# Optimization experiments

Hardware: AMD Instinct MI355X
Metric: run time of the kernel (lower is better)

Reference implementation:

```python
import jax, jax.numpy as jnp
import numpy as np

B, S, H = 1, 2048, 1024
NH, NKV, HD = 16, 4, 64  # n_attn_heads, n_kv_heads, head_dim


def setup_inputs() -> dict:
    key = jax.random.key(0)
    k1, k2, k3, k4 = jax.random.split(key, 4)
    x = jax.random.normal(k1, (B, S, H), dtype=jnp.float32)
    Wq = jax.random.normal(k2, (H, H), dtype=jnp.float32) * 0.02
    Wk = jax.random.normal(k3, (NKV * HD, H), dtype=jnp.float32) * 0.02
    Wv = jax.random.normal(k4, (NKV * HD, H), dtype=jnp.float32) * 0.02
    return {"x": x, "Wq": Wq, "Wk": Wk, "Wv": Wv}


def reference(x, Wq, Wk, Wv):
    b, s, h = x.shape
    rep = NH // NKV
    # projections (torch Linear: x @ W.T)
    q = (x @ Wq.T).reshape(b, s, NH, HD).transpose(0, 2, 1, 3)      # [b, NH, s, d]
    k = (x @ Wk.T).reshape(b, s, NKV, HD).transpose(0, 2, 1, 3)     # [b, NKV, s, d]
    v = (x @ Wv.T).reshape(b, s, NKV, HD).transpose(0, 2, 1, 3)
    # repeat_kv: expand each kv head rep times
    k = jnp.repeat(k, rep, axis=1)                                   # [b, NH, s, d]
    v = jnp.repeat(v, rep, axis=1)
    # NOTE: source scales by 1/sqrt(hidden_size), not 1/sqrt(head_dim)
    scale = 1.0 / np.sqrt(H).astype(np.float32)
    scores = jnp.einsum('bhqd,bhkd->bhqk', q, k) * scale             # [b, NH, s, s]
    causal = jnp.tril(jnp.ones((s, s), dtype=bool))
    scores = jnp.where(causal[None, None], scores, -jnp.inf)
    probs = jax.nn.softmax(scores, axis=-1)
    y = jnp.einsum('bhqk,bhkd->bhqd', probs, v)                      # [b, NH, s, d]
    return y.transpose(0, 2, 1, 3).reshape(b, s, NH * HD)
```

## Files before the change

### kernel.cpp

```cpp
#include <hip/hip_runtime.h>

#define S_LEN 2048
#define HID   1024
#define NHEAD 16
#define NKVH  4
#define HDIM  64
#define NPROJ 1536
#define QKSTR 1280

typedef __bf16 bf16x8 __attribute__((ext_vector_type(8)));
typedef __bf16 bf16x4 __attribute__((ext_vector_type(4)));
typedef float  f32x4  __attribute__((ext_vector_type(4)));

typedef const __attribute__((address_space(1))) void* gas_ptr;
typedef __attribute__((address_space(3))) void*       las_ptr;

#define QSCALE 0.04508422f

__device__ __forceinline__ unsigned short f2bf(float f) {
    unsigned u = __builtin_bit_cast(unsigned, f);
    u = u + 0x7FFFu + ((u >> 16) & 1u);
    return (unsigned short)(u >> 16);
}

__global__ __launch_bounds__(256) void cvt_all(
    const float* __restrict__ x,  const float* __restrict__ wq,
    const float* __restrict__ wk, const float* __restrict__ wv,
    unsigned short* __restrict__ xbf, unsigned short* __restrict__ wbf)
{
    const long nx  = (long)S_LEN * HID;
    const long nwq = (long)HID * HID;
    const long nwk = (long)256 * HID;
    long i = (long)(blockIdx.x * 256 + threadIdx.x) * 4;
    const float* src; unsigned short* dst;
    if (i < nx)                  { src = x  + i;                 dst = xbf + i; }
    else if (i < nx + nwq)       { long j = i - nx;              src = wq + j; dst = wbf + j; }
    else if (i < nx + nwq + nwk) { long j = i - nx - nwq;        src = wk + j; dst = wbf + nwq + j; }
    else                         { long j = i - nx - nwq - nwk;  src = wv + j; dst = wbf + nwq + nwk + j; }
    float4 v = *(const float4*)src;
    ushort4 o; o.x = f2bf(v.x); o.y = f2bf(v.y); o.z = f2bf(v.z); o.w = f2bf(v.w);
    *(ushort4*)dst = o;
}

__global__ __launch_bounds__(256, 2) void proj_gemm(
    const unsigned short* __restrict__ xbf,
    const unsigned short* __restrict__ wbf,
    unsigned short* __restrict__ qkv,
    unsigned short* __restrict__ vT)
{
    __shared__ unsigned short At[2][64 * 64];
    __shared__ unsigned short Bt[2][96 * 64];
    const int tid = threadIdx.x;
    const int w = tid >> 6, l = tid & 63;
    const int quad = l >> 4, lane16 = l & 15;
    const int m0 = blockIdx.y * 64, n0 = blockIdx.x * 96;
    const int wm = (w & 1) * 32, wn = (w >> 1) * 48;

    const int srow = l >> 3;
    const int scol = ((l & 7) ^ srow) * 8;

    f32x4 acc[2][3] = {};

    #define STAGE(KT, BUF)                                                              \
        do {                                                                            \
            _Pragma("unroll")                                                           \
            for (int c = 0; c < 2; ++c) {                                               \
                const int rbase = w * 16 + c * 8;                                       \
                const unsigned short* ga =                                              \
                    xbf + (long)(m0 + rbase + srow) * HID + (KT) + scol;                \
                __builtin_amdgcn_global_load_lds((gas_ptr)ga,                           \
                    (las_ptr)&At[BUF][rbase * 64], 16, 0, 0);                           \
            }                                                                           \
            _Pragma("unroll")                                                           \
            for (int c = 0; c < 3; ++c) {                                               \
                const int rbase = w * 24 + c * 8;                                       \
                const unsigned short* gb =                                              \
                    wbf + (long)(n0 + rbase + srow) * HID + (KT) + scol;                \
                __builtin_amdgcn_global_load_lds((gas_ptr)gb,                           \
                    (las_ptr)&Bt[BUF][rbase * 64], 16, 0, 0);                           \
            }                                                                           \
        } while (0)

    STAGE(0, 0);

    for (int i = 0; i < 16; ++i) {
        const int cur = i & 1;
        __syncthreads();
        if (i + 1 < 16) STAGE((i + 1) * 64, cur ^ 1);

        #pragma unroll
        for (int ks = 0; ks < 2; ++ks) {
            const int swz = ((ks * 4 + quad) ^ (lane16 & 7)) * 8;
            bf16x8 a[2], b[3];
            #pragma unroll
            for (int mi = 0; mi < 2; ++mi)
                a[mi] = *(const bf16x8*)&At[cur][(wm + mi * 16 + lane16) * 64 + swz];
            #pragma unroll
            for (int ni = 0; ni < 3; ++ni)
                b[ni] = *(const bf16x8*)&Bt[cur][(wn + ni * 16 + lane16) * 64 + swz];
            #pragma unroll
            for (int mi = 0; mi < 2; ++mi)
                #pragma unroll
                for (int ni = 0; ni < 3; ++ni)
                    acc[mi][ni] = __builtin_amdgcn_mfma_f32_16x16x32_bf16(a[mi], b[ni], acc[mi][ni], 0, 0, 0);
        }
    }
    #undef STAGE

    #pragma unroll
    for (int mi = 0; mi < 2; ++mi) {
        const int row = m0 + wm + mi * 16 + quad * 4;
        #pragma unroll
        for (int ni = 0; ni < 3; ++ni) {
            const int col = n0 + wn + ni * 16 + lane16;
            #pragma unroll
            for (int r = 0; r < 4; ++r) {
                const float v = acc[mi][ni][r];
                if (col < 1024)
                    qkv[(long)(row + r) * QKSTR + col] = f2bf(v * QSCALE);
                else if (col < 1280)
                    qkv[(long)(row + r) * QKSTR + col] = f2bf(v);
                else
                    vT[(long)(col - 1280) * S_LEN + (row + r)] = f2bf(v);
            }
        }
    }
}

#define KSTR 72
__global__ __launch_bounds__(256) void attn(
    const unsigned short* __restrict__ qkv,
    const unsigned short* __restrict__ vT,
    float* __restrict__ out)
{
    __shared__ unsigned short Kt[2][64 * KSTR];
    __shared__ unsigned short Vt[2][64 * KSTR];
    __shared__ unsigned short Pb[4 * 16 * KSTR];

    const int tid = threadIdx.x;
    const int w = tid >> 6, l = tid & 63;
    const int quad = l >> 4, lane16 = l & 15;
    const int bx = blockIdx.x, by = blockIdx.y;
    const int qt = (by & 8) ? (31 - bx) : bx;
    const int h  = by;
    const int kh = h >> 2;
    const int qcol = h * 64;
    const int kcol = 1024 + kh * 64;

    const long qrow = (long)(qt * 64 + w * 16 + lane16);
    bf16x8 qa0 = *(const bf16x8*)&qkv[qrow * QKSTR + qcol + quad * 8];
    bf16x8 qa1 = *(const bf16x8*)&qkv[qrow * QKSTR + qcol + 32 + quad * 8];

    f32x4 o[4] = {};
    float rsum[4] = {0.f, 0.f, 0.f, 0.f};

    unsigned short* pw = &Pb[w * 16 * KSTR];

    const int sr = tid >> 2, ss = tid & 3;
    const long vrow = (long)(kh * 64 + sr) * S_LEN;

    bf16x8 kr0, kr1, vr0, vr1;
    {
        const long gk = (long)sr * QKSTR + kcol + ss * 16;
        kr0 = *(const bf16x8*)&qkv[gk];
        kr1 = *(const bf16x8*)&qkv[gk + 8];
        const long gv = vrow + ss * 16;
        vr0 = *(const bf16x8*)&vT[gv];
        vr1 = *(const bf16x8*)&vT[gv + 8];
    }

    for (int kt = 0; kt <= qt; ++kt) {
        const int cur = kt & 1;
        *(bf16x8*)&Kt[cur][sr * KSTR + ss * 16]     = kr0;
        *(bf16x8*)&Kt[cur][sr * KSTR + ss * 16 + 8] = kr1;
        *(bf16x8*)&Vt[cur][sr * KSTR + ss * 16]     = vr0;
        *(bf16x8*)&Vt[cur][sr * KSTR + ss * 16 + 8] = vr1;
        if (kt < qt) {
            const long gk = (long)((kt + 1) * 64 + sr) * QKSTR + kcol + ss * 16;
            kr0 = *(const bf16x8*)&qkv[gk];
            kr1 = *(const bf16x8*)&qkv[gk + 8];
            const long gv = vrow + (kt + 1) * 64 + ss * 16;
            vr0 = *(const bf16x8*)&vT[gv];
            vr1 = *(const bf16x8*)&vT[gv + 8];
        }
        __syncthreads();

        f32x4 sacc[4] = {};
        #pragma unroll
        for (int t = 0; t < 4; ++t) {
            bf16x8 kb0 = *(const bf16x8*)&Kt[cur][(t * 16 + lane16) * KSTR + quad * 8];
            bf16x8 kb1 = *(const bf16x8*)&Kt[cur][(t * 16 + lane16) * KSTR + 32 + quad * 8];
            sacc[t] = __builtin_amdgcn_mfma_f32_16x16x32_bf16(kb0, qa0, sacc[t], 0, 0, 0);
            sacc[t] = __builtin_amdgcn_mfma_f32_16x16x32_bf16(kb1, qa1, sacc[t], 0, 0, 0);
        }

        if (kt == qt) {
            #pragma unroll
            for (int t = 0; t < 4; ++t) {
                const int kvw = t * 16 + quad * 4;
                #pragma unroll
                for (int r = 0; r < 4; ++r)
                    if (kvw + r > w * 16 + lane16) sacc[t][r] = -3.0e38f;
            }
        }

        #pragma unroll
        for (int t = 0; t < 4; ++t) {
            const float p0 = __builtin_amdgcn_exp2f(sacc[t][0]);
            const float p1 = __builtin_amdgcn_exp2f(sacc[t][1]);
            const float p2 = __builtin_amdgcn_exp2f(sacc[t][2]);
            const float p3 = __builtin_amdgcn_exp2f(sacc[t][3]);
            rsum[t] += (p0 + p1) + (p2 + p3);
            bf16x4 pk;
            pk[0] = (__bf16)p0; pk[1] = (__bf16)p1;
            pk[2] = (__bf16)p2; pk[3] = (__bf16)p3;
            *(bf16x4*)&pw[lane16 * KSTR + ((t * 16 + quad * 4) ^ ((lane16 & 12) << 1))] = pk;
        }

        asm volatile("" ::: "memory");
        __builtin_amdgcn_sched_barrier(0);

        #pragma unroll
        for (int ks = 0; ks < 2; ++ks) {
            bf16x8 pa = *(const bf16x8*)&pw[lane16 * KSTR + ((ks * 32 + quad * 8) ^ ((lane16 & 12) << 1))];
            #pragma unroll
            for (int t = 0; t < 4; ++t) {
                bf16x8 vb = *(const bf16x8*)&Vt[cur][(t * 16 + lane16) * KSTR + ks * 32 + quad * 8];
                o[t] = __builtin_amdgcn_mfma_f32_16x16x32_bf16(pa, vb, o[t], 0, 0, 0);
            }
        }
    }

    float total = (rsum[0] + rsum[1]) + (rsum[2] + rsum[3]);
    total += __shfl_xor(total, 16);
    total += __shfl_xor(total, 32);
    const float invt = 1.0f / total;
    float inv[4];
    #pragma unroll
    for (int r = 0; r < 4; ++r)
        inv[r] = __shfl(invt, quad * 4 + r);

    const int orow = qt * 64 + w * 16 + quad * 4;
    #pragma unroll
    for (int t = 0; t < 4; ++t) {
        const int col = h * 64 + t * 16 + lane16;
        #pragma unroll
        for (int r = 0; r < 4; ++r)
            out[(long)(orow + r) * (NHEAD * HDIM) + col] = o[t][r] * inv[r];
    }
}

extern "C" void kernel_launch(void* const* d_in, const int* in_sizes, int n_in,
                              void* d_out, int out_size, void* d_ws, size_t ws_size,
                              hipStream_t stream) {
    const float* x  = (const float*)d_in[0];
    const float* wq = (const float*)d_in[1];
    const float* wk = (const float*)d_in[2];
    const float* wv = (const float*)d_in[3];
    float* out = (float*)d_out;

    unsigned short* xbf = (unsigned short*)d_ws;
    unsigned short* wbf = xbf + (size_t)S_LEN * HID;
    unsigned short* qkv = wbf + (size_t)NPROJ * HID;
    unsigned short* vT  = qkv + (size_t)S_LEN * QKSTR;

    cvt_all<<<dim3(3584), dim3(256), 0, stream>>>(x, wq, wk, wv, xbf, wbf);
    proj_gemm<<<dim3(16, 32), dim3(256), 0, stream>>>(xbf, wbf, qkv, vT);
    attn<<<dim3(32, 16), dim3(256), 0, stream>>>(qkv, vT, out);
}
```

Measured before the change: 114.0 us.

## Load K/V fragments directly from global into registers, dropping LDS staging

The attention kernel no longer stages K and V tiles through double-buffered shared memory with block-wide barriers. Each wave now loads its MFMA operand fragments for K and V straight from global memory into registers, prefetching the next tile after the current tile's MFMAs. It also raises wave priority around the MFMA blocks and adds an occupancy hint to launch bounds. This removes the __syncthreads and the LDS traffic, but each of the four waves re-reads the same K/V data from global or L2 instead of sharing one copy, and register pressure rises.

Measured after the change: 151.0 us. +32.4%, slower.

```diff
diff --git a/kernel.cpp b/kernel.cpp
--- a/kernel.cpp
+++ b/kernel.cpp
@@ -128,13 +128,11 @@
 }
 
 #define KSTR 72
-__global__ __launch_bounds__(256) void attn(
+__global__ __launch_bounds__(256, 2) void attn(
     const unsigned short* __restrict__ qkv,
     const unsigned short* __restrict__ vT,
     float* __restrict__ out)
 {
-    __shared__ unsigned short Kt[2][64 * KSTR];
-    __shared__ unsigned short Vt[2][64 * KSTR];
     __shared__ unsigned short Pb[4 * 16 * KSTR];
 
     const int tid = threadIdx.x;
@@ -156,43 +154,47 @@
 
     unsigned short* pw = &Pb[w * 16 * KSTR];
 
-    const int sr = tid >> 2, ss = tid & 3;
-    const long vrow = (long)(kh * 64 + sr) * S_LEN;
-
-    bf16x8 kr0, kr1, vr0, vr1;
-    {
-        const long gk = (long)sr * QKSTR + kcol + ss * 16;
-        kr0 = *(const bf16x8*)&qkv[gk];
-        kr1 = *(const bf16x8*)&qkv[gk + 8];
-        const long gv = vrow + ss * 16;
-        vr0 = *(const bf16x8*)&vT[gv];
-        vr1 = *(const bf16x8*)&vT[gv + 8];
-    }
+    const unsigned short* kbase = qkv + kcol;
+    const unsigned short* vbase = vT + (long)(kh * 64) * S_LEN;
+
+    bf16x8 kb[8], vb[8];
+
+    #define LOADK(KT)                                                                   \
+        do {                                                                            \
+            _Pragma("unroll")                                                           \
+            for (int t = 0; t < 4; ++t) {                                               \
+                const long gr = (long)((KT) * 64 + t * 16 + lane16) * QKSTR;            \
+                kb[2 * t]     = *(const bf16x8*)&kbase[gr + quad * 8];                  \
+                kb[2 * t + 1] = *(const bf16x8*)&kbase[gr + 32 + quad * 8];             \
+            }                                                                           \
+        } while (0)
+
+    #define LOADV(KT)                                                                   \
+        do {                                                                            \
+            _Pragma("unroll")                                                           \
+            for (int ks = 0; ks < 2; ++ks)                                              \
+                _Pragma("unroll")                                                       \
+                for (int t = 0; t < 4; ++t) {                                           \
+                    const long gv = (long)(t * 16 + lane16) * S_LEN +                   \
+                                    (KT) * 64 + ks * 32 + quad * 8;                     \
+                    vb[ks * 4 + t] = *(const bf16x8*)&vbase[gv];                        \
+                }                                                                       \
+        } while (0)
+
+    LOADK(0);
+    LOADV(0);
 
     for (int kt = 0; kt <= qt; ++kt) {
-        const int cur = kt & 1;
-        *(bf16x8*)&Kt[cur][sr * KSTR + ss * 16]     = kr0;
-        *(bf16x8*)&Kt[cur][sr * KSTR + ss * 16 + 8] = kr1;
-        *(bf16x8*)&Vt[cur][sr * KSTR + ss * 16]     = vr0;
-        *(bf16x8*)&Vt[cur][sr * KSTR + ss * 16 + 8] = vr1;
-        if (kt < qt) {
-            const long gk = (long)((kt + 1) * 64 + sr) * QKSTR + kcol + ss * 16;
-            kr0 = *(const bf16x8*)&qkv[gk];
-            kr1 = *(const bf16x8*)&qkv[gk + 8];
-            const long gv = vrow + (kt + 1) * 64 + ss * 16;
-            vr0 = *(const bf16x8*)&vT[gv];
-            vr1 = *(const bf16x8*)&vT[gv + 8];
-        }
-        __syncthreads();
-
         f32x4 sacc[4] = {};
+        __builtin_amdgcn_s_setprio(1);
         #pragma unroll
         for (int t = 0; t < 4; ++t) {
-            bf16x8 kb0 = *(const bf16x8*)&Kt[cur][(t * 16 + lane16) * KSTR + quad * 8];
-            bf16x8 kb1 = *(const bf16x8*)&Kt[cur][(t * 16 + lane16) * KSTR + 32 + quad * 8];
-            sacc[t] = __builtin_amdgcn_mfma_f32_16x16x32_bf16(kb0, qa0, sacc[t], 0, 0, 0);
-            sacc[t] = __builtin_amdgcn_mfma_f32_16x16x32_bf16(kb1, qa1, sacc[t], 0, 0, 0);
-        }
+            sacc[t] = __builtin_amdgcn_mfma_f32_16x16x32_bf16(kb[2 * t],     qa0, sacc[t], 0, 0, 0);
+            sacc[t] = __builtin_amdgcn_mfma_f32_16x16x32_bf16(kb[2 * t + 1], qa1, sacc[t], 0, 0, 0);
+        }
+        __builtin_amdgcn_s_setprio(0);
+
+        if (kt < qt) LOADK(kt + 1);
 
         if (kt == qt) {
             #pragma unroll
@@ -220,16 +222,21 @@
         asm volatile("" ::: "memory");
         __builtin_amdgcn_sched_barrier(0);
 
-        #pragma unroll
-        for (int ks = 0; ks < 2; ++ks) {
-            bf16x8 pa = *(const bf16x8*)&pw[lane16 * KSTR + ((ks * 32 + quad * 8) ^ ((lane16 & 12) << 1))];
-            #pragma unroll
-            for (int t = 0; t < 4; ++t) {
-                bf16x8 vb = *(const bf16x8*)&Vt[cur][(t * 16 + lane16) * KSTR + ks * 32 + quad * 8];
-                o[t] = __builtin_amdgcn_mfma_f32_16x16x32_bf16(pa, vb, o[t], 0, 0, 0);
-            }
-        }
-    }
+        bf16x8 pa0 = *(const bf16x8*)&pw[lane16 * KSTR + ((quad * 8)      ^ ((lane16 & 12) << 1))];
+        bf16x8 pa1 = *(const bf16x8*)&pw[lane16 * KSTR + ((32 + quad * 8) ^ ((lane16 & 12) << 1))];
+        __builtin_amdgcn_s_setprio(1);
+        #pragma unroll
+        for (int t = 0; t < 4; ++t)
+            o[t] = __builtin_amdgcn_mfma_f32_16x16x32_bf16(pa0, vb[t], o[t], 0, 0, 0);
+        #pragma unroll
+        for (int t = 0; t < 4; ++t)
+            o[t] = __builtin_amdgcn_mfma_f32_16x16x32_bf16(pa1, vb[4 + t], o[t], 0, 0, 0);
+        __builtin_amdgcn_s_setprio(0);
+
+        if (kt < qt) LOADV(kt + 1);
+    }
+    #undef LOADK
+    #undef LOADV
 
     float total = (rsum[0] + rsum[1]) + (rsum[2] + rsum[3]);
     total += __shfl_xor(total, 16);
```

## Pass attention probabilities via lane shuffles instead of LDS round-trip

Applied to the files above, without the earlier changes.

Replaces the per-wave shared-memory staging of the bf16 probability tile with cross-lane shuffles that rebuild the MFMA A-operand layout directly in registers. This removes the LDS buffer, its writes and reads, and the scheduling barrier. It also raises MFMA issue priority around the two matmul phases and adds a min-blocks hint of 3 to launch bounds. The cost is 16 shuffles per tile plus selects, more register pressure, and a register cap from the occupancy hint.

Measured after the change: 115.8 us. About the same (+1.6%).

```diff
diff --git a/kernel.cpp b/kernel.cpp
--- a/kernel.cpp
+++ b/kernel.cpp
@@ -10,7 +10,9 @@
 
 typedef __bf16 bf16x8 __attribute__((ext_vector_type(8)));
 typedef __bf16 bf16x4 __attribute__((ext_vector_type(4)));
+typedef __bf16 bf16x2 __attribute__((ext_vector_type(2)));
 typedef float  f32x4  __attribute__((ext_vector_type(4)));
+typedef unsigned u32x4 __attribute__((ext_vector_type(4)));
 
 typedef const __attribute__((address_space(1))) void* gas_ptr;
 typedef __attribute__((address_space(3))) void*       las_ptr;
@@ -128,14 +130,13 @@
 }
 
 #define KSTR 72
-__global__ __launch_bounds__(256) void attn(
+__global__ __launch_bounds__(256, 3) void attn(
     const unsigned short* __restrict__ qkv,
     const unsigned short* __restrict__ vT,
     float* __restrict__ out)
 {
     __shared__ unsigned short Kt[2][64 * KSTR];
     __shared__ unsigned short Vt[2][64 * KSTR];
-    __shared__ unsigned short Pb[4 * 16 * KSTR];
 
     const int tid = threadIdx.x;
     const int w = tid >> 6, l = tid & 63;
@@ -154,10 +155,12 @@
     f32x4 o[4] = {};
     float rsum[4] = {0.f, 0.f, 0.f, 0.f};
 
-    unsigned short* pw = &Pb[w * 16 * KSTR];
-
     const int sr = tid >> 2, ss = tid & 3;
     const long vrow = (long)(kh * 64 + sr) * S_LEN;
+
+    const int srcA = lane16 + ((l & 16) << 1);
+    const int srcB = srcA + 16;
+    const bool up = (l >= 32);
 
     bf16x8 kr0, kr1, vr0, vr1;
     {
@@ -186,6 +189,7 @@
         __syncthreads();
 
         f32x4 sacc[4] = {};
+        __builtin_amdgcn_s_setprio(1);
         #pragma unroll
         for (int t = 0; t < 4; ++t) {
             bf16x8 kb0 = *(const bf16x8*)&Kt[cur][(t * 16 + lane16) * KSTR + quad * 8];
@@ -193,6 +197,7 @@
             sacc[t] = __builtin_amdgcn_mfma_f32_16x16x32_bf16(kb0, qa0, sacc[t], 0, 0, 0);
             sacc[t] = __builtin_amdgcn_mfma_f32_16x16x32_bf16(kb1, qa1, sacc[t], 0, 0, 0);
         }
+        __builtin_amdgcn_s_setprio(0);
 
         if (kt == qt) {
             #pragma unroll
@@ -204,6 +209,7 @@
             }
         }
 
+        unsigned h8[8];
         #pragma unroll
         for (int t = 0; t < 4; ++t) {
             const float p0 = __builtin_amdgcn_exp2f(sacc[t][0]);
@@ -211,24 +217,39 @@
             const float p2 = __builtin_amdgcn_exp2f(sacc[t][2]);
             const float p3 = __builtin_amdgcn_exp2f(sacc[t][3]);
             rsum[t] += (p0 + p1) + (p2 + p3);
-            bf16x4 pk;
-            pk[0] = (__bf16)p0; pk[1] = (__bf16)p1;
-            pk[2] = (__bf16)p2; pk[3] = (__bf16)p3;
-            *(bf16x4*)&pw[lane16 * KSTR + ((t * 16 + quad * 4) ^ ((lane16 & 12) << 1))] = pk;
-        }
-
-        asm volatile("" ::: "memory");
-        __builtin_amdgcn_sched_barrier(0);
-
-        #pragma unroll
-        for (int ks = 0; ks < 2; ++ks) {
-            bf16x8 pa = *(const bf16x8*)&pw[lane16 * KSTR + ((ks * 32 + quad * 8) ^ ((lane16 & 12) << 1))];
-            #pragma unroll
-            for (int t = 0; t < 4; ++t) {
-                bf16x8 vb = *(const bf16x8*)&Vt[cur][(t * 16 + lane16) * KSTR + ks * 32 + quad * 8];
-                o[t] = __builtin_amdgcn_mfma_f32_16x16x32_bf16(pa, vb, o[t], 0, 0, 0);
-            }
-        }
+            bf16x2 lo, hi;
+            lo[0] = (__bf16)p0; lo[1] = (__bf16)p1;
+            hi[0] = (__bf16)p2; hi[1] = (__bf16)p3;
+            h8[t * 2]     = __builtin_bit_cast(unsigned, lo);
+            h8[t * 2 + 1] = __builtin_bit_cast(unsigned, hi);
+        }
+
+        unsigned sA[8], sB[8];
+        #pragma unroll
+        for (int i = 0; i < 8; ++i) {
+            sA[i] = __shfl(h8[i], srcA);
+            sB[i] = __shfl(h8[i], srcB);
+        }
+        u32x4 w0, w1;
+        w0[0] = up ? sA[2] : sA[0];  w0[1] = up ? sA[3] : sA[1];
+        w0[2] = up ? sB[2] : sB[0];  w0[3] = up ? sB[3] : sB[1];
+        w1[0] = up ? sA[6] : sA[4];  w1[1] = up ? sA[7] : sA[5];
+        w1[2] = up ? sB[6] : sB[4];  w1[3] = up ? sB[7] : sB[5];
+        const bf16x8 pa0 = __builtin_bit_cast(bf16x8, w0);
+        const bf16x8 pa1 = __builtin_bit_cast(bf16x8, w1);
+
+        __builtin_amdgcn_s_setprio(1);
+        #pragma unroll
+        for (int t = 0; t < 4; ++t) {
+            bf16x8 vb0 = *(const bf16x8*)&Vt[cur][(t * 16 + lane16) * KSTR + quad * 8];
+            o[t] = __builtin_amdgcn_mfma_f32_16x16x32_bf16(pa0, vb0, o[t], 0, 0, 0);
+        }
+        #pragma unroll
+        for (int t = 0; t < 4; ++t) {
+            bf16x8 vb1 = *(const bf16x8*)&Vt[cur][(t * 16 + lane16) * KSTR + 32 + quad * 8];
+            o[t] = __builtin_amdgcn_mfma_f32_16x16x32_bf16(pa1, vb1, o[t], 0, 0, 0);
+        }
+        __builtin_amdgcn_s_setprio(0);
     }
 
     float total = (rsum[0] + rsum[1]) + (rsum[2] + rsum[3]);
```

## Keep P in registers and compute transposed PV with 16x16x16 MFMA

Applied to the files above, without the earlier changes.

The attention kernel stops staging the softmax probabilities through shared memory. The S accumulator layout is reused directly as the B operand of 16x16x16 bf16 MFMAs computing O^T = V^T·P^T, so each lane keeps its P fragment in registers. This removes the LDS write/read round trip and the per-wave P buffer, and it lets the output normalisation use a per-lane inverse with no shuffles. In exchange it issues twice as many smaller MFMAs and narrower V reads from LDS. It also adds s_setprio around the MFMA sections and a launch bound hint of two blocks per CU.

After: 115.8 us. About the same (+1.6%).

```diff
diff --git a/kernel.cpp b/kernel.cpp
--- a/kernel.cpp
+++ b/kernel.cpp
@@ -11,6 +11,7 @@
 typedef __bf16 bf16x8 __attribute__((ext_vector_type(8)));
 typedef __bf16 bf16x4 __attribute__((ext_vector_type(4)));
 typedef float  f32x4  __attribute__((ext_vector_type(4)));
+typedef short  s16x4  __attribute__((ext_vector_type(4)));
 
 typedef const __attribute__((address_space(1))) void* gas_ptr;
 typedef __attribute__((address_space(3))) void*       las_ptr;
@@ -21,6 +22,17 @@
     unsigned u = __builtin_bit_cast(unsigned, f);
     u = u + 0x7FFFu + ((u >> 16) & 1u);
     return (unsigned short)(u >> 16);
+}
+
+__device__ __forceinline__ f32x4 mfma_16x16x16_bf16(s16x4 a, s16x4 b, f32x4 c) {
+#if __has_builtin(__builtin_amdgcn_mfma_f32_16x16x16bf16_1k)
+    return __builtin_amdgcn_mfma_f32_16x16x16bf16_1k(a, b, c, 0, 0, 0);
+#else
+    f32x4 d = c;
+    asm volatile("s_nop 1\n\tv_mfma_f32_16x16x16_bf16 %0, %1, %2, %0\n\ts_nop 3"
+                 : "+v"(d) : "v"(a), "v"(b));
+    return d;
+#endif
 }
 
 __global__ __launch_bounds__(256) void cvt_all(
@@ -128,14 +140,13 @@
 }
 
 #define KSTR 72
-__global__ __launch_bounds__(256) void attn(
+__global__ __launch_bounds__(256, 2) void attn(
     const unsigned short* __restrict__ qkv,
     const unsigned short* __restrict__ vT,
     float* __restrict__ out)
 {
     __shared__ unsigned short Kt[2][64 * KSTR];
     __shared__ unsigned short Vt[2][64 * KSTR];
-    __shared__ unsigned short Pb[4 * 16 * KSTR];
 
     const int tid = threadIdx.x;
     const int w = tid >> 6, l = tid & 63;
@@ -151,10 +162,8 @@
     bf16x8 qa0 = *(const bf16x8*)&qkv[qrow * QKSTR + qcol + quad * 8];
     bf16x8 qa1 = *(const bf16x8*)&qkv[qrow * QKSTR + qcol + 32 + quad * 8];
 
-    f32x4 o[4] = {};
+    f32x4 oT[4] = {};
     float rsum[4] = {0.f, 0.f, 0.f, 0.f};
-
-    unsigned short* pw = &Pb[w * 16 * KSTR];
 
     const int sr = tid >> 2, ss = tid & 3;
     const long vrow = (long)(kh * 64 + sr) * S_LEN;
@@ -186,6 +195,7 @@
         __syncthreads();
 
         f32x4 sacc[4] = {};
+        __builtin_amdgcn_s_setprio(1);
         #pragma unroll
         for (int t = 0; t < 4; ++t) {
             bf16x8 kb0 = *(const bf16x8*)&Kt[cur][(t * 16 + lane16) * KSTR + quad * 8];
@@ -193,6 +203,7 @@
             sacc[t] = __builtin_amdgcn_mfma_f32_16x16x32_bf16(kb0, qa0, sacc[t], 0, 0, 0);
             sacc[t] = __builtin_amdgcn_mfma_f32_16x16x32_bf16(kb1, qa1, sacc[t], 0, 0, 0);
         }
+        __builtin_amdgcn_s_setprio(0);
 
         if (kt == qt) {
             #pragma unroll
@@ -204,6 +215,7 @@
             }
         }
 
+        s16x4 pfrag[4];
         #pragma unroll
         for (int t = 0; t < 4; ++t) {
             const float p0 = __builtin_amdgcn_exp2f(sacc[t][0]);
@@ -214,39 +226,32 @@
             bf16x4 pk;
             pk[0] = (__bf16)p0; pk[1] = (__bf16)p1;
             pk[2] = (__bf16)p2; pk[3] = (__bf16)p3;
-            *(bf16x4*)&pw[lane16 * KSTR + ((t * 16 + quad * 4) ^ ((lane16 & 12) << 1))] = pk;
-        }
-
-        asm volatile("" ::: "memory");
-        __builtin_amdgcn_sched_barrier(0);
-
-        #pragma unroll
-        for (int ks = 0; ks < 2; ++ks) {
-            bf16x8 pa = *(const bf16x8*)&pw[lane16 * KSTR + ((ks * 32 + quad * 8) ^ ((lane16 & 12) << 1))];
+            pfrag[t] = __builtin_bit_cast(s16x4, pk);
+        }
+
+        __builtin_amdgcn_s_setprio(1);
+        #pragma unroll
+        for (int dt = 0; dt < 4; ++dt)
             #pragma unroll
             for (int t = 0; t < 4; ++t) {
-                bf16x8 vb = *(const bf16x8*)&Vt[cur][(t * 16 + lane16) * KSTR + ks * 32 + quad * 8];
-                o[t] = __builtin_amdgcn_mfma_f32_16x16x32_bf16(pa, vb, o[t], 0, 0, 0);
+                bf16x4 va = *(const bf16x4*)&Vt[cur][(dt * 16 + lane16) * KSTR + t * 16 + quad * 4];
+                oT[dt] = mfma_16x16x16_bf16(__builtin_bit_cast(s16x4, va), pfrag[t], oT[dt]);
             }
-        }
+        __builtin_amdgcn_s_setprio(0);
     }
 
     float total = (rsum[0] + rsum[1]) + (rsum[2] + rsum[3]);
     total += __shfl_xor(total, 16);
     total += __shfl_xor(total, 32);
     const float invt = 1.0f / total;
-    float inv[4];
+
+    const long orow_q = (long)(qt * 64 + w * 16 + lane16);
     #pragma unroll
-    for (int r = 0; r < 4; ++r)
-        inv[r] = __shfl(invt, quad * 4 + r);
-
-    const int orow = qt * 64 + w * 16 + quad * 4;
-    #pragma unroll
-    for (int t = 0; t < 4; ++t) {
-        const int col = h * 64 + t * 16 + lane16;
+    for (int dt = 0; dt < 4; ++dt) {
+        const int col = h * 64 + dt * 16 + quad * 4;
         #pragma unroll
         for (int r = 0; r < 4; ++r)
-            out[(long)(orow + r) * (NHEAD * HDIM) + col] = o[t][r] * inv[r];
+            out[orow_q * (NHEAD * HDIM) + col + r] = oT[dt][r] * invt;
     }
 }
 
```
